# Performance work log

Hardware: AMD Instinct MI355X
Metric: run time of the kernel (lower is better)

## Reference

```python
import jax, jax.numpy as jnp
import numpy as np

H, DN, DR, DV = 16, 128, 64, 128   # heads, nope dim, rope dim, v dim
QR, KR = 1536, 512                 # q / kv lora ranks
HI, DI, TOPK = 32, 128, 512        # indexer heads, indexer head dim, index_topk

def rmsnorm(x, w, eps=1e-6):
    return x * jax.lax.rsqrt(jnp.mean(x * x, -1, keepdims=True) + eps) * w

def layernorm(x, w, b, eps=1e-5):
    m = jnp.mean(x, -1, keepdims=True)
    v = jnp.mean((x - m) ** 2, -1, keepdims=True)
    return (x - m) * jax.lax.rsqrt(v + eps) * w + b

def rope_interleaved(x, cos, sin):
    # x: [b,s,h,d]; cos,sin: [s,d//2]; pairs are (x[2j], x[2j+1])
    x0, x1 = x[..., 0::2], x[..., 1::2]
    c, s = cos[None, :, None, :], sin[None, :, None, :]
    return jnp.stack([x0 * c - x1 * s, x0 * s + x1 * c], -1).reshape(x.shape)

def rope_half(x, cos, sin):
    # non-interleaved variant: pairs are (x[j], x[j+d/2]); output = [real_half, imag_half]
    d = x.shape[-1] // 2
    x0, x1 = x[..., :d], x[..., d:]
    c, s = cos[None, :, None, :], sin[None, :, None, :]
    return jnp.concatenate([x0 * c - x1 * s, x0 * s + x1 * c], -1)

def setup_inputs():
    key = jax.random.key(0)
    B, S, DM = 1, 2048, 2048
    ks = jax.random.split(key, 10)
    w = lambda k, shape: jax.random.normal(k, shape, jnp.float32) * 0.02
    inp = {
        'hidden_states': jax.random.normal(ks[0], (B, S, DM), jnp.float32),
        'wq_a': w(ks[1], (QR, DM)),
        'q_norm_w': jnp.ones((QR,), jnp.float32),
        'wq_b': w(ks[2], (H * (DN + DR), QR)),
        'wkv_a': w(ks[3], (KR + DR, DM)),
        'kv_norm_w': jnp.ones((KR,), jnp.float32),
        'wkv_b': w(ks[4], (H * (DN + DV), KR)),
        'wo': w(ks[5], (DM, H * DV)),
        'idx_wq_b': w(ks[6], (HI * DI, QR)),
        'idx_wk': w(ks[7], (DI, DM)),
        'idx_kn_w': jnp.ones((DI,), jnp.float32),
        'idx_kn_b': jnp.zeros((DI,), jnp.float32),
        'idx_wproj': w(ks[8], (HI, DM)),
    }
    ang = jnp.arange(S, dtype=jnp.float32)[:, None] / (10000.0 ** (jnp.arange(0, DR, 2, dtype=jnp.float32) / DR))[None, :]
    inp['freqs_cos'], inp['freqs_sin'] = jnp.cos(ang), jnp.sin(ang)
    inp['mask'] = jnp.broadcast_to(
        jnp.where(jnp.tril(jnp.ones((S, S), bool)), 0.0, -jnp.inf).astype(jnp.float32), (B, S, S))
    return inp

def reference(hidden_states, freqs_cos, freqs_sin, mask, wq_a, q_norm_w, wq_b, wkv_a,
              kv_norm_w, wkv_b, wo, idx_wq_b, idx_wk, idx_kn_w, idx_kn_b, idx_wproj):
    B, S, DM = hidden_states.shape
    # --- MLA low-rank Q/KV projections ---
    qr = rmsnorm(hidden_states @ wq_a.T, q_norm_w)                       # [B,S,QR]
    q = (qr @ wq_b.T).reshape(B, S, H, DN + DR)
    q_pe = rope_interleaved(q[..., DN:], freqs_cos, freqs_sin)
    q = jnp.concatenate([q[..., :DN], q_pe], -1)                         # [B,S,H,192]
    kv_all = hidden_states @ wkv_a.T                                     # [B,S,KR+DR]
    kv = rmsnorm(kv_all[..., :KR], kv_norm_w)
    k_pe = rope_interleaved(kv_all[..., KR:][:, :, None, :], freqs_cos, freqs_sin)  # [B,S,1,DR]
    kvp = (kv @ wkv_b.T).reshape(B, S, H, DN + DV)
    k = jnp.concatenate([kvp[..., :DN], jnp.broadcast_to(k_pe, (B, S, H, DR))], -1)
    v = kvp[..., DN:]                                                    # [B,S,H,DV]
    scores = jnp.einsum('bshd,bthd->bsht', q, k) * (DN + DR) ** -0.5
    # --- indexer: relu-weighted scores -> top-k token set ---
    qi = (qr @ idx_wq_b.T).reshape(B, S, HI, DI)
    qi = jnp.concatenate([rope_half(qi[..., :DR], freqs_cos, freqs_sin), qi[..., DR:]], -1)
    ki = layernorm(hidden_states @ idx_wk.T, idx_kn_w, idx_kn_b)         # [B,S,DI]
    ki_pe = rope_half(ki[..., :DR][:, :, None, :], freqs_cos, freqs_sin)[:, :, 0, :]
    ki = jnp.concatenate([ki_pe, ki[..., DR:]], -1)
    wts = (hidden_states @ idx_wproj.T) * HI ** -0.5                     # [B,S,HI]
    iscores = jax.nn.relu(jnp.einsum('bshd,btd->bsht', qi, ki) * DI ** -0.5) * wts[..., None]
    index_scores = iscores.sum(2) + mask                                 # [B,S,S]
    topk_idx = jax.lax.top_k(index_scores, TOPK)[1]                      # [B,S,TOPK]
    index_mask = jnp.full((B, S, S), -jnp.inf, jnp.float32)
    index_mask = index_mask.at[jnp.arange(B)[:, None, None],
                               jnp.arange(S)[None, :, None], topk_idx].set(0.0)
    # --- sparse-masked attention ---
    scores = scores + (index_mask + mask)[:, :, None, :]
    probs = jax.nn.softmax(scores, axis=-1)
    out = jnp.einsum('bsht,bthd->bshd', probs, v).reshape(B, S, H * DV)
    return out @ wo.T
```

## Files before the change

kernel.cpp:

```cpp
#include <hip/hip_runtime.h>
#include <stdint.h>

typedef unsigned int uint;
typedef unsigned short u16;
typedef unsigned long long u64;

typedef float  f32x4 __attribute__((ext_vector_type(4)));
typedef uint   u32x4 __attribute__((ext_vector_type(4)));
typedef u16    u16x4 __attribute__((ext_vector_type(4)));
typedef u16    u16x8 __attribute__((ext_vector_type(8)));
typedef __bf16 bf16x8 __attribute__((ext_vector_type(8)));

#define DEV static __device__ __forceinline__
#define MFMA(a,b,c) __builtin_amdgcn_mfma_f32_16x16x32_bf16((a),(b),(c),0,0,0)
#define GLDS(src,dst) __builtin_amdgcn_global_load_lds((const __attribute__((address_space(1))) void*)(src),(__attribute__((address_space(3))) void*)(dst),16,0,0)

DEV u16 f2bf(float x){ union{float f;uint u;} v; v.f=x; return (u16)((v.u + 0x7fffu + ((v.u>>16)&1u))>>16); }
DEV float bf2f(u16 b){ union{uint u;float f;} v; v.u=((uint)b)<<16; return v.f; }
DEV int imin(int a,int b){ return a<b?a:b; }

__global__ void cvt_all(
    const float* __restrict__ hs, const float* __restrict__ wqa, const float* __restrict__ iwqb,
    const float* __restrict__ iwk, const float* __restrict__ iwp,
    const float* __restrict__ wqbw, const float* __restrict__ wkva, const float* __restrict__ wkvb,
    const float* __restrict__ wow,
    u16* __restrict__ hid_hi, u16* __restrict__ hid_lo, u16* __restrict__ wqa_hi, u16* __restrict__ wqa_lo,
    u16* __restrict__ iwqb_hi, u16* __restrict__ iwqb_lo, u16* __restrict__ kiwp_hi, u16* __restrict__ kiwp_lo,
    u16* __restrict__ wqb_b, u16* __restrict__ wkva_b, u16* __restrict__ wkvb_b, u16* __restrict__ wo_b)
{
  int i = blockIdx.x*blockDim.x + threadIdx.x;
  int st = gridDim.x*blockDim.x;
  for(; i < 6537216; i += st){
    const float* src; u16 *dh, *dl=nullptr; int j; bool split;
    if(i < 1048576){ src=hs;   dh=hid_hi;  dl=hid_lo;  j=i;         split=true; }
    else if(i < 1835008){ src=wqa;  dh=wqa_hi;  dl=wqa_lo;  j=i-1048576; split=true; }
    else if(i < 3407872){ src=iwqb; dh=iwqb_hi; dl=iwqb_lo; j=i-1835008; split=true; }
    else if(i < 3473408){ src=iwk;  dh=kiwp_hi; dl=kiwp_lo; j=i-3407872; split=true; }
    else if(i < 3489792){ src=iwp;  dh=kiwp_hi+128*2048; dl=kiwp_lo+128*2048; j=i-3473408; split=true; }
    else if(i < 4669440){ src=wqbw; dh=wqb_b;  j=i-3489792; split=false; }
    else if(i < 4964352){ src=wkva; dh=wkva_b; j=i-4669440; split=false; }
    else if(i < 5488640){ src=wkvb; dh=wkvb_b; j=i-4964352; split=false; }
    else               { src=wow;  dh=wo_b;   j=i-5488640; split=false; }
    f32x4 x = reinterpret_cast<const f32x4*>(src)[j];
    u16x4 h;
    #pragma unroll
    for(int k=0;k<4;k++) h[k]=f2bf(x[k]);
    reinterpret_cast<u16x4*>(dh)[j]=h;
    if(split){
      u16x4 l;
      #pragma unroll
      for(int k=0;k<4;k++) l[k]=f2bf(x[k]-bf2f(h[k]));
      reinterpret_cast<u16x4*>(dl)[j]=l;
    }
  }
}

template<int BK>
DEV void stageT(const u16* __restrict__ gbase, int ld, int row0, int maxrow, int k0, u16* lds){
  int tid = threadIdx.x, w = tid>>6, l = tid&63;
  if(BK==32){
    #pragma unroll
    for(int j=0;j<2;j++){
      int seg = w + j*4;
      int row = seg*16 + (l>>2);
      int gr = row0 + row; if(gr > maxrow) gr = maxrow;
      GLDS(gbase + (size_t)gr*ld + k0 + (l&3)*8, lds + seg*512);
    }
  } else {
    #pragma unroll
    for(int j=0;j<4;j++){
      int c = w + j*4;
      int row = c*8 + (l>>3);
      int gr = row0 + row; if(gr > maxrow) gr = maxrow;
      GLDS(gbase + (size_t)gr*ld + k0 + (l&7)*8, lds + c*512);
    }
  }
}

template<int SPLIT, int BK>
__global__ __launch_bounds__(256,2) void gemm_glds(
    const u16* __restrict__ Ah, const u16* __restrict__ Al, int lda,
    const u16* __restrict__ Bh, const u16* __restrict__ Bl, int ldb,
    float* __restrict__ C, int ldc, int M, int N, int K)
{
  __shared__ u16 sAh[128*BK];
  __shared__ u16 sBh[128*BK];
  __shared__ u16 sAl[SPLIT?128*BK:8];
  __shared__ u16 sBl[SPLIT?128*BK:8];
  const int tid = threadIdx.x;
  const int w = tid>>6, l = tid&63;
  const int wr = w>>1, wc = w&1;
  const int l15 = l&15, l16 = l>>4;

  int gx = gridDim.x;
  int nwg = gx*gridDim.y;
  int orig = blockIdx.x + gx*blockIdx.y;
  int qq = nwg>>3, rr = nwg&7, xc = orig&7, oo = orig>>3;
  int wg = (xc<rr ? xc*(qq+1) : rr*(qq+1)+(xc-rr)*qq) + oo;
  int m0 = (wg/gx)*128, n0 = (wg%gx)*128;

  int kz = K/(int)gridDim.z;
  int kbeg = blockIdx.z*kz;

  f32x4 acc[4][4];
  #pragma unroll
  for(int m=0;m<4;m++)
    #pragma unroll
    for(int n=0;n<4;n++) acc[m][n] = f32x4{0.f,0.f,0.f,0.f};

  for(int k0=kbeg; k0<kbeg+kz; k0+=BK){
    __syncthreads();
    stageT<BK>(Ah, lda, m0, M-1, k0, sAh);
    stageT<BK>(Bh, ldb, n0, N-1, k0, sBh);
    if(SPLIT){
      stageT<BK>(Al, lda, m0, M-1, k0, sAl);
      stageT<BK>(Bl, ldb, n0, N-1, k0, sBl);
    }
    asm volatile("s_waitcnt vmcnt(0)" ::: "memory");
    __syncthreads();
    #pragma unroll
    for(int kk=0;kk<BK/32;kk++){
      bf16x8 ah[4], bh[4];
      #pragma unroll
      for(int m=0;m<4;m++) ah[m] = *reinterpret_cast<const bf16x8*>(&sAh[(wr*64+m*16+l15)*BK + kk*32 + l16*8]);
      #pragma unroll
      for(int n=0;n<4;n++) bh[n] = *reinterpret_cast<const bf16x8*>(&sBh[(wc*64+n*16+l15)*BK + kk*32 + l16*8]);
      #pragma unroll
      for(int m=0;m<4;m++)
        #pragma unroll
        for(int n=0;n<4;n++) acc[m][n] = MFMA(ah[m], bh[n], acc[m][n]);
      if(SPLIT){
        bf16x8 t[4];
        #pragma unroll
        for(int n=0;n<4;n++) t[n] = *reinterpret_cast<const bf16x8*>(&sBl[(wc*64+n*16+l15)*BK + kk*32 + l16*8]);
        #pragma unroll
        for(int m=0;m<4;m++)
          #pragma unroll
          for(int n=0;n<4;n++) acc[m][n] = MFMA(ah[m], t[n], acc[m][n]);
        #pragma unroll
        for(int m=0;m<4;m++) t[m] = *reinterpret_cast<const bf16x8*>(&sAl[(wr*64+m*16+l15)*BK + kk*32 + l16*8]);
        #pragma unroll
        for(int m=0;m<4;m++)
          #pragma unroll
          for(int n=0;n<4;n++) acc[m][n] = MFMA(t[m], bh[n], acc[m][n]);
      }
    }
  }
  float* Cp = C + (size_t)blockIdx.z*M*ldc;
  #pragma unroll
  for(int m=0;m<4;m++){
    int row = m0 + wr*64 + m*16 + l16*4;
    #pragma unroll
    for(int n=0;n<4;n++){
      int col = n0 + wc*64 + n*16 + l15;
      if(col < N){
        #pragma unroll
        for(int r=0;r<4;r++){
          int rrow = row + r;
          if(rrow < M) Cp[(size_t)rrow*ldc + col] = acc[m][n][r];
        }
      }
    }
  }
}

__global__ __launch_bounds__(256) void rmsnorm_qr_split(
    const float* __restrict__ in, const float* __restrict__ w,
    u16* __restrict__ hi, u16* __restrict__ lo)
{
  int s = blockIdx.x, tid = threadIdx.x;
  __shared__ float red[4];
  const float* x = in + (size_t)s*1536;
  const size_t plane = 2048ull*1536;
  float xv[6]; float ss=0.f;
  #pragma unroll
  for(int i=0;i<6;i++){ int c = tid+i*256; xv[i] = x[c] + x[plane+c]; ss += xv[i]*xv[i]; }
  #pragma unroll
  for(int o=32;o>0;o>>=1) ss += __shfl_down(ss,o,64);
  if((tid&63)==0) red[tid>>6]=ss;
  __syncthreads();
  float total = red[0]+red[1]+red[2]+red[3];
  float scale = rsqrtf(total*(1.0f/1536.0f) + 1e-6f);
  #pragma unroll
  for(int i=0;i<6;i++){
    int c = tid + i*256;
    float vv = xv[i]*scale*w[c];
    u16 hv = f2bf(vv);
    hi[(size_t)s*1536+c]=hv;
    lo[(size_t)s*1536+c]=f2bf(vv - bf2f(hv));
  }
}

__global__ __launch_bounds__(256) void kv_norm_rope(
    const float* __restrict__ kva, const float* __restrict__ w,
    const float* __restrict__ fcos, const float* __restrict__ fsin,
    u16* __restrict__ kvb, float* __restrict__ kpe)
{
  int s = blockIdx.x, tid = threadIdx.x;
  __shared__ float red[4];
  const size_t plane = 2048ull*576;
  float xv[2]={0.f,0.f};
  #pragma unroll
  for(int c=0;c<4;c++){
    const float* xp = kva + (size_t)c*plane + (size_t)s*576;
    xv[0]+=xp[tid]; xv[1]+=xp[tid+256];
  }
  float ss = xv[0]*xv[0]+xv[1]*xv[1];
  #pragma unroll
  for(int o=32;o>0;o>>=1) ss += __shfl_down(ss,o,64);
  if((tid&63)==0) red[tid>>6]=ss;
  __syncthreads();
  float total = red[0]+red[1]+red[2]+red[3];
  float scale = rsqrtf(total*(1.0f/512.0f)+1e-6f);
  #pragma unroll
  for(int i=0;i<2;i++){ int c=tid+i*256; kvb[(size_t)s*512+c]=f2bf(xv[i]*scale*w[c]); }
  if(tid<32){
    float x0=0.f, x1=0.f;
    #pragma unroll
    for(int c=0;c<4;c++){
      const float* xp = kva + (size_t)c*plane + (size_t)s*576;
      x0 += xp[512+2*tid]; x1 += xp[513+2*tid];
    }
    float c0=fcos[(size_t)s*32+tid], s_=fsin[(size_t)s*32+tid];
    kpe[(size_t)s*64+2*tid]   = x0*c0 - x1*s_;
    kpe[(size_t)s*64+2*tid+1] = x0*s_ + x1*c0;
  }
}

__global__ __launch_bounds__(256) void rope_q_cvt(const float* __restrict__ qpre,
    const float* __restrict__ fcos, const float* __restrict__ fsin, u16* __restrict__ qb)
{
  int s = blockIdx.x;
  const float* rowp = qpre + (size_t)s*3072;
  u16* op = qb + (size_t)s*3072;
  for(int idx=threadIdx.x; idx<3072; idx+=256){
    int hh = idx/192, d = idx - hh*192;
    float vv;
    if(d < 128) vv = rowp[hh*192 + d];
    else{
      int i2 = (d-128)>>1;
      float c0 = fcos[(size_t)s*32+i2], s_ = fsin[(size_t)s*32+i2];
      float x0 = rowp[hh*192 + 128 + 2*i2], x1 = rowp[hh*192 + 129 + 2*i2];
      vv = ((d&1)==0) ? (x0*c0 - x1*s_) : (x0*s_ + x1*c0);
    }
    op[idx] = f2bf(vv);
  }
}

__global__ __launch_bounds__(256) void qi_rope_split(const float* __restrict__ qpre,
    const float* __restrict__ fcos, const float* __restrict__ fsin,
    u16* __restrict__ hi, u16* __restrict__ lo)
{
  int s = blockIdx.x;
  const float* rowp = qpre + (size_t)s*4096;
  for(int idx=threadIdx.x; idx<4096; idx+=256){
    int hh = idx>>7, d = idx&127;
    const float* hb = rowp + (hh<<7);
    float vv;
    if(d<32){ float c0=fcos[(size_t)s*32+d], s_=fsin[(size_t)s*32+d]; vv = hb[d]*c0 - hb[d+32]*s_; }
    else if(d<64){ int i2=d-32; float c0=fcos[(size_t)s*32+i2], s_=fsin[(size_t)s*32+i2]; vv = hb[i2]*s_ + hb[d]*c0; }
    else vv = hb[d];
    u16 hv = f2bf(vv);
    hi[(size_t)s*4096+idx]=hv;
    lo[(size_t)s*4096+idx]=f2bf(vv - bf2f(hv));
  }
}

__global__ __launch_bounds__(128) void ki_ln_rope_split(
    const float* __restrict__ kpre, const float* __restrict__ w, const float* __restrict__ bb,
    const float* __restrict__ fcos, const float* __restrict__ fsin,
    u16* __restrict__ hi, u16* __restrict__ lo, float* __restrict__ wts_out)
{
  int s = blockIdx.x, tid = threadIdx.x;
  __shared__ float red[2];
  __shared__ float ybuf[128];
  const size_t plane = 2048ull*160;
  float x = 0.f;
  #pragma unroll
  for(int c=0;c<8;c++) x += kpre[(size_t)c*plane + (size_t)s*160 + tid];
  if(tid<32){
    float ws = 0.f;
    #pragma unroll
    for(int c=0;c<8;c++) ws += kpre[(size_t)c*plane + (size_t)s*160 + 128 + tid];
    wts_out[(size_t)s*160 + 128 + tid] = ws;
  }
  float v = x;
  #pragma unroll
  for(int o=32;o>0;o>>=1) v += __shfl_down(v,o,64);
  if((tid&63)==0) red[tid>>6]=v;
  __syncthreads();
  float mean = (red[0]+red[1])*(1.f/128.f);
  __syncthreads();
  float dx = x - mean;
  v = dx*dx;
  #pragma unroll
  for(int o=32;o>0;o>>=1) v += __shfl_down(v,o,64);
  if((tid&63)==0) red[tid>>6]=v;
  __syncthreads();
  float var = (red[0]+red[1])*(1.f/128.f);
  float y = dx*rsqrtf(var+1e-5f)*w[tid] + bb[tid];
  ybuf[tid]=y;
  __syncthreads();
  float r;
  if(tid<32){ float c0=fcos[(size_t)s*32+tid], s_=fsin[(size_t)s*32+tid]; r = ybuf[tid]*c0 - ybuf[tid+32]*s_; }
  else if(tid<64){ int i2=tid-32; float c0=fcos[(size_t)s*32+i2], s_=fsin[(size_t)s*32+i2]; r = ybuf[i2]*s_ + ybuf[tid]*c0; }
  else r = y;
  u16 hv=f2bf(r);
  hi[(size_t)s*128+tid]=hv;
  lo[(size_t)s*128+tid]=f2bf(r-bf2f(hv));
}

__global__ __launch_bounds__(256) void transpose_assemble(const float* __restrict__ kvp,
    const float* __restrict__ kpe, u16* __restrict__ vt, u16* __restrict__ kb){
  __shared__ u16 T[64*136];
  int s0 = blockIdx.x*64, h = blockIdx.y;
  int tid = threadIdx.x;
  for(int idx=tid; idx<64*192; idx+=256){
    int r = idx/192, d = idx - r*192;
    float val = (d<128) ? kvp[(size_t)(s0+r)*4096 + h*256 + d] : kpe[(size_t)(s0+r)*64 + (d-128)];
    kb[((size_t)(s0+r)*16 + h)*192 + d] = f2bf(val);
  }
  #pragma unroll
  for(int i=0;i<8;i++){
    int ch = i*256 + tid;
    int r = ch>>5, cc = ch&31;
    f32x4 x = *reinterpret_cast<const f32x4*>(&kvp[(size_t)(s0+r)*4096 + h*256 + 128 + cc*4]);
    u16x4 y;
    #pragma unroll
    for(int j=0;j<4;j++) y[j] = f2bf(x[j]);
    *reinterpret_cast<u16x4*>(&T[r*136 + cc*4]) = y;
  }
  __syncthreads();
  #pragma unroll
  for(int i=0;i<4;i++){
    int ch = i*256 + tid;
    int d = ch>>3, sc = ch&7;
    u16x8 y;
    #pragma unroll
    for(int j=0;j<8;j++) y[j] = T[(sc*8+j)*136 + d];
    *reinterpret_cast<u16x8*>(&vt[((size_t)h*128 + d)*2048 + s0 + sc*8]) = y;
  }
}

DEV void isc_pass128(const u16* __restrict__ Q, const u16* __restrict__ Kb,
                     f32x4 (&sc)[4][2], int wm, int wn, int l15, int l16){
  #pragma unroll
  for(int ks=0;ks<4;ks++){
    bf16x8 a[4], b[2];
    #pragma unroll
    for(int m=0;m<4;m++){
      int row = wm*64 + m*16 + l15;
      a[m] = *reinterpret_cast<const bf16x8*>(&Q[row*128 + ((((ks<<2)+l16) ^ (row&7))<<3)]);
    }
    #pragma unroll
    for(int n=0;n<2;n++){
      int row = wn*32 + n*16 + l15;
      b[n] = *reinterpret_cast<const bf16x8*>(&Kb[row*128 + ((((ks<<2)+l16) ^ (row&7))<<3)]);
    }
    #pragma unroll
    for(int m=0;m<4;m++)
      #pragma unroll
      for(int n=0;n<2;n++) sc[m][n] = MFMA(a[m], b[n], sc[m][n]);
  }
}

__global__ __launch_bounds__(512,2) void idx_scores6(
    const u16* __restrict__ qih, const u16* __restrict__ qil,
    const u16* __restrict__ kih, const u16* __restrict__ kil,
    const float* __restrict__ wts,
    float* __restrict__ p0, float* __restrict__ p1, float* __restrict__ p2, float* __restrict__ p3)
{
  __shared__ u16 Kh[128*128];
  __shared__ u16 Kl[128*128];
  __shared__ u16 Qb[2][128*128];
  __shared__ float Wl[128*9];
  int orig = blockIdx.x;
  int bid = (orig&7)*68 + (orig>>3);
  int tileIdx = bid>>2, hg = bid&3;
  int si=0, t=tileIdx;
  while(t >= si+1){ t -= si+1; si++; }
  int s0 = si*128, t0 = t*128;
  float* plane = (hg==0)?p0:(hg==1)?p1:(hg==2)?p2:p3;
  float* outp = plane + (size_t)tileIdx*16384;
  int h0 = hg*8;
  int tid=threadIdx.x, w=tid>>6, l=tid&63;
  int wm=w>>2, wn=w&3, l15=l&15, l16=l>>4;
  const float cscale = 0.015625f;
  #pragma unroll
  for(int rnd=0;rnd<4;rnd++){
    int cid = rnd*512 + w*64 + l;
    int row = cid>>4, cc = cid&15;
    int scc = cc ^ (row&7);
    GLDS(kih + (size_t)(t0+row)*128 + scc*8, Kh + rnd*4096 + w*512);
    GLDS(kil + (size_t)(t0+row)*128 + scc*8, Kl + rnd*4096 + w*512);
  }
  #pragma unroll
  for(int rnd=0;rnd<4;rnd++){
    int cid = rnd*512 + w*64 + l;
    int row = cid>>4, cc = cid&15;
    int scc = cc ^ (row&7);
    GLDS(qih + (size_t)(s0+row)*4096 + h0*128 + scc*8, Qb[0] + rnd*4096 + w*512);
  }
  #pragma unroll
  for(int it=0;it<2;it++){
    int idx = it*512 + tid;
    int row = idx>>3, hh = idx&7;
    Wl[row*9+hh] = wts[(size_t)(s0+row)*160 + 128 + h0 + hh]*cscale;
  }
  asm volatile("s_waitcnt vmcnt(0)" ::: "memory");
  __syncthreads();
  f32x4 accI[4][2], sc[4][2];
  #pragma unroll
  for(int m=0;m<4;m++) for(int n=0;n<2;n++) accI[m][n] = f32x4{0.f,0.f,0.f,0.f};
  for(int s=0;s<16;s++){
    int nxt = s+1;
    if(nxt < 16){
      const u16* src = (nxt&1) ? qil : qih;
      int hh = h0 + (nxt>>1);
      u16* dst = Qb[nxt&1];
      #pragma unroll
      for(int rnd=0;rnd<4;rnd++){
        int cid = rnd*512 + w*64 + l;
        int row = cid>>4, cc = cid&15;
        int scc = cc ^ (row&7);
        GLDS(src + (size_t)(s0+row)*4096 + hh*128 + scc*8, dst + rnd*4096 + w*512);
      }
    }
    const u16* Q = Qb[s&1];
    if((s&1)==0){
      #pragma unroll
      for(int m=0;m<4;m++) for(int n=0;n<2;n++) sc[m][n] = f32x4{0.f,0.f,0.f,0.f};
      isc_pass128(Q, Kh, sc, wm, wn, l15, l16);
      isc_pass128(Q, Kl, sc, wm, wn, l15, l16);
    } else {
      isc_pass128(Q, Kh, sc, wm, wn, l15, l16);
      int hh = s>>1;
      #pragma unroll
      for(int m=0;m<4;m++)
        #pragma unroll
        for(int r=0;r<4;r++){
          float wv = Wl[(wm*64+m*16+l16*4+r)*9 + hh];
          #pragma unroll
          for(int n=0;n<2;n++) accI[m][n][r] += fmaxf(sc[m][n][r],0.f)*wv;
        }
    }
    asm volatile("s_waitcnt vmcnt(0)" ::: "memory");
    __syncthreads();
  }
  #pragma unroll
  for(int m=0;m<4;m++)
    #pragma unroll
    for(int n=0;n<2;n++)
      #pragma unroll
      for(int r=0;r<4;r++)
        outp[(wm*64+m*16+l16*4+r)*128 + wn*32 + n*16 + l15] = accI[m][n][r];
}

DEV uint fkey(float f){ union{float f;uint u;} v; v.f=f; return (v.u & 0x80000000u) ? ~v.u : (v.u | 0x80000000u); }

__global__ __launch_bounds__(256) void topk_mask(
    const float* __restrict__ p0, const float* __restrict__ p1,
    const float* __restrict__ p2, const float* __restrict__ p3, u64* __restrict__ bits)
{
  int s = blockIdx.x;
  int n = s+1;
  int tid = threadIdx.x;
  if(n <= 512){
    for(int wI=tid; wI<32; wI+=256){
      u64 m=0; int base=wI*64;
      if(base < n){ int cnt=n-base; m = (cnt>=64)? ~0ull : ((1ull<<cnt)-1ull); }
      bits[(size_t)s*32+wI]=m;
    }
    return;
  }
  __shared__ float row[2048];
  __shared__ uint hist[256];
  __shared__ uint sh_B, sh_k;
  __shared__ uint wcnt[32];
  int si = s>>7, sr = s&127;
  size_t triBase = (size_t)(si*(si+1)/2);
  for(int c=tid; c<n; c+=256){
    size_t off = (triBase + (size_t)(c>>7))*16384 + (size_t)sr*128 + (c&127);
    row[c] = p0[off]+p1[off]+p2[off]+p3[off];
  }
  __syncthreads();
  uint prefix=0, k=512;
  for(int shift=24; shift>=0; shift-=8){
    hist[tid]=0;
    __syncthreads();
    for(int t2=tid;t2<n;t2+=256){
      uint u = fkey(row[t2]);
      bool ok = (shift==24) || ((u>>(shift+8)) == (prefix>>(shift+8)));
      if(ok) atomicAdd(&hist[(u>>shift)&255u],1u);
    }
    __syncthreads();
    for(int offd=1; offd<256; offd<<=1){
      uint add = (tid+offd<256)? hist[tid+offd] : 0u;
      __syncthreads();
      hist[tid] += add;
      __syncthreads();
    }
    uint nxtv = (tid<255)? hist[tid+1] : 0u;
    if(hist[tid]>=k && nxtv<k){ sh_B=(uint)tid; sh_k = k - nxtv; }
    __syncthreads();
    prefix |= sh_B<<shift;
    k = sh_k;
    __syncthreads();
  }
  uint thr = prefix;
  if(tid<32) wcnt[tid]=0;
  __syncthreads();
  int nw = (n+63)>>6;
  if(tid < nw){
    int base=tid*64, end = base+64; if(end>n) end=n;
    uint c=0;
    for(int t2=base;t2<end;t2++) if(fkey(row[t2])==thr) c++;
    wcnt[tid]=c;
  }
  __syncthreads();
  if(tid==0){
    uint runv=0;
    for(int i=0;i<32;i++){ uint c=wcnt[i]; wcnt[i]=runv; runv+=c; }
  }
  __syncthreads();
  if(tid<32){
    u64 m=0; int base=tid*64;
    if(base<n){
      uint rank = wcnt[tid];
      int end = base+64; if(end>n) end=n;
      for(int t2=base;t2<end;t2++){
        uint u = fkey(row[t2]);
        if(u>thr) m |= (1ull<<(t2-base));
        else if(u==thr){ if(rank<k) m |= (1ull<<(t2-base)); rank++; }
      }
    }
    bits[(size_t)s*32+tid]=m;
  }
}

__global__ __launch_bounds__(256,3) void flash_attn(
    const u16* __restrict__ q, const u16* __restrict__ k, const u16* __restrict__ vt,
    const u64* __restrict__ bits, u16* __restrict__ o,
    u16* __restrict__ Opart, float* __restrict__ ml)
{
  __shared__ u16 Ks[64*192];
  __shared__ u16 Vt[128*64];
  __shared__ u16 Pl[64*72];
  int h = blockIdx.y;
  int pp = blockIdx.x;
  int sblk=0, chunk=0;
  for(int i=0;i<32;i++){
    int sb = 31-i; int ncc = (sb>>3)+1;
    if(pp < ncc){ sblk=sb; chunk=pp; break; }
    pp -= ncc;
  }
  int nc = (sblk>>3)+1, ntiles = sblk+1, s0 = sblk*64;
  int tid=threadIdx.x, w=tid>>6, l=tid&63;
  int l15=l&15, l16=l>>4;
  const float sscale = 0.07216878364870323f;
  bf16x8 qf[6];
  #pragma unroll
  for(int ks=0;ks<6;ks++)
    qf[ks] = *reinterpret_cast<const bf16x8*>(&q[((size_t)(s0+w*16+l15)*16 + h)*192 + ks*32 + l16*8]);
  f32x4 Oa[8];
  #pragma unroll
  for(int n=0;n<8;n++) Oa[n] = f32x4{0.f,0.f,0.f,0.f};
  float mrun[4], lrun[4];
  #pragma unroll
  for(int r=0;r<4;r++){ mrun[r]=-__builtin_inff(); lrun[r]=0.f; }
  int tt0 = chunk*8, tt1 = imin(tt0+8, ntiles);
  for(int tt=tt0; tt<tt1; tt++){
    int t0 = tt*64;
    __syncthreads();
    #pragma unroll
    for(int rnd=0;rnd<6;rnd++){
      int cid = rnd*256 + w*64 + l;
      int row = cid/24, cc = cid - row*24;
      int scc = cc ^ (row&7);
      GLDS(k + ((size_t)(t0+row)*16 + h)*192 + scc*8, Ks + rnd*2048 + w*512);
    }
    #pragma unroll
    for(int rnd=0;rnd<4;rnd++){
      int cid = rnd*256 + w*64 + l;
      int row = cid>>3, cc = cid&7;
      int scc = cc ^ (row&7);
      GLDS(vt + ((size_t)h*128 + row)*2048 + t0 + scc*8, Vt + rnd*2048 + w*512);
    }
    asm volatile("s_waitcnt vmcnt(0)" ::: "memory");
    __syncthreads();
    f32x4 S[4];
    #pragma unroll
    for(int n=0;n<4;n++) S[n] = f32x4{0.f,0.f,0.f,0.f};
    #pragma unroll
    for(int ks=0;ks<6;ks++){
      bf16x8 b[4];
      #pragma unroll
      for(int n=0;n<4;n++){
        int row = n*16+l15;
        b[n] = *reinterpret_cast<const bf16x8*>(&Ks[row*192 + ((((ks<<2)+l16) ^ (row&7))<<3)]);
      }
      #pragma unroll
      for(int n=0;n<4;n++) S[n] = MFMA(qf[ks], b[n], S[n]);
    }
    #pragma unroll
    for(int r=0;r<4;r++){
      int srow = s0 + w*16 + l16*4 + r;
      u64 wrd = bits[(size_t)srow*32 + (t0>>6)];
      float mx = -__builtin_inff();
      #pragma unroll
      for(int n=0;n<4;n++){
        int bitp = n*16 + l15;
        int tcol = t0 + bitp;
        bool ok = (tcol <= srow) && ((wrd>>bitp)&1ull);
        float val = ok ? S[n][r]*sscale : -__builtin_inff();
        S[n][r] = val;
        mx = fmaxf(mx, val);
      }
      #pragma unroll
      for(int off=1;off<16;off<<=1) mx = fmaxf(mx, __shfl_xor(mx, off, 64));
      float mold = mrun[r];
      float mnew = fmaxf(mold, mx);
      bool inf0 = (mnew == -__builtin_inff());
      float alpha = inf0 ? 1.f : __expf(mold - mnew);
      float rs = 0.f;
      #pragma unroll
      for(int n=0;n<4;n++){
        float p = inf0 ? 0.f : __expf(S[n][r] - mnew);
        S[n][r] = p;
        rs += p;
      }
      #pragma unroll
      for(int off=1;off<16;off<<=1) rs += __shfl_xor(rs, off, 64);
      mrun[r]=mnew;
      lrun[r] = lrun[r]*alpha + rs;
      #pragma unroll
      for(int n=0;n<8;n++) Oa[n][r] *= alpha;
    }
    #pragma unroll
    for(int n=0;n<4;n++)
      #pragma unroll
      for(int r=0;r<4;r++)
        Pl[(w*16+l16*4+r)*72 + n*16+l15] = f2bf(S[n][r]);
    #pragma unroll
    for(int ks=0;ks<2;ks++){
      bf16x8 a = *reinterpret_cast<const bf16x8*>(&Pl[(w*16+l15)*72 + ks*32 + l16*8]);
      bf16x8 bb[8];
      #pragma unroll
      for(int n=0;n<8;n++){
        int d = n*16+l15;
        bb[n] = *reinterpret_cast<const bf16x8*>(&Vt[d*64 + ((((ks<<2)+l16) ^ (d&7))<<3)]);
      }
      #pragma unroll
      for(int n=0;n<8;n++) Oa[n] = MFMA(a, bb[n], Oa[n]);
    }
  }
  if(nc == 1){
    #pragma unroll
    for(int r=0;r<4;r++){
      int srow = s0 + w*16 + l16*4 + r;
      float inv = 1.f/lrun[r];
      #pragma unroll
      for(int n=0;n<8;n++)
        o[(size_t)srow*2048 + h*128 + n*16 + l15] = f2bf(Oa[n][r]*inv);
    }
  } else {
    int part = ((h*32 + sblk)<<2) + chunk;
    u16* Op = Opart + (size_t)part*8192;
    #pragma unroll
    for(int r=0;r<4;r++){
      int rit = w*16 + l16*4 + r;
      #pragma unroll
      for(int n=0;n<8;n++)
        Op[rit*128 + n*16 + l15] = f2bf(Oa[n][r]);
      if(l15==0){
        ml[(size_t)part*128 + rit*2]   = mrun[r];
        ml[(size_t)part*128 + rit*2+1] = lrun[r];
      }
    }
  }
}

__global__ __launch_bounds__(256) void flash_combine(
    const u16* __restrict__ Opart, const float* __restrict__ ml, u16* __restrict__ o)
{
  int b = blockIdx.x;
  int h = b/24, sblk = 8 + (b%24);
  int nc = (sblk>>3)+1;
  int tid = threadIdx.x;
  int r = tid>>2, dq = (tid&3)*32;
  int s0 = sblk*64;
  int pbase = (h*32+sblk)<<2;
  float m[4], lv[4], wgt[4];
  float M = -__builtin_inff();
  for(int c=0;c<nc;c++){
    m[c]  = ml[(size_t)(pbase+c)*128 + r*2];
    lv[c] = ml[(size_t)(pbase+c)*128 + r*2 + 1];
    if(lv[c] > 0.f) M = fmaxf(M, m[c]);
  }
  float L = 0.f;
  for(int c=0;c<nc;c++){
    wgt[c] = (lv[c] > 0.f) ? __expf(m[c]-M) : 0.f;
    L += lv[c]*wgt[c];
  }
  float inv = 1.f/L;
  for(int dd=0; dd<32; dd+=8){
    float accv[8];
    #pragma unroll
    for(int j=0;j<8;j++) accv[j]=0.f;
    for(int c=0;c<nc;c++){
      u16x8 pv = *reinterpret_cast<const u16x8*>(&Opart[(size_t)(pbase+c)*8192 + r*128 + dq + dd]);
      #pragma unroll
      for(int j=0;j<8;j++) accv[j] += wgt[c]*bf2f(pv[j]);
    }
    u16x8 ov;
    #pragma unroll
    for(int j=0;j<8;j++) ov[j] = f2bf(accv[j]*inv);
    *reinterpret_cast<u16x8*>(&o[(size_t)(s0+r)*2048 + h*128 + dq + dd]) = ov;
  }
}

extern "C" void kernel_launch(void* const* d_in, const int* in_sizes, int n_in,
                              void* d_out, int out_size, void* d_ws, size_t ws_size,
                              hipStream_t stream)
{
  (void)in_sizes; (void)n_in; (void)out_size;
  const float* hs   = (const float*)d_in[0];
  const float* wqa  = (const float*)d_in[1];
  const float* qnw  = (const float*)d_in[2];
  const float* wqbw = (const float*)d_in[3];
  const float* wkva = (const float*)d_in[4];
  const float* kvnw = (const float*)d_in[5];
  const float* wkvb = (const float*)d_in[6];
  const float* wow  = (const float*)d_in[7];
  const float* iwqb = (const float*)d_in[8];
  const float* iwk  = (const float*)d_in[9];
  const float* iknw = (const float*)d_in[10];
  const float* iknb = (const float*)d_in[11];
  const float* iwp  = (const float*)d_in[12];
  const float* fcos = (const float*)d_in[13];
  const float* fsin = (const float*)d_in[14];
  float* outp = (float*)d_out;

  char* base = (char*)d_ws;
  size_t off = 0;
  auto alloc = [&](size_t bytes)->char*{ char* p = base+off; off += (bytes+255)&~(size_t)255; return p; };
  u16* hid_hi = (u16*)alloc(2048ull*2048*2);
  u16* hid_lo = (u16*)alloc(2048ull*2048*2);
  u16* wqa_hi = (u16*)alloc(1536ull*2048*2);
  u16* wqa_lo = (u16*)alloc(1536ull*2048*2);
  u16* wqb_b  = (u16*)alloc(3072ull*1536*2);
  u16* wkva_b = (u16*)alloc(576ull*2048*2);
  u16* wkvb_b = (u16*)alloc(4096ull*512*2);
  u16* wo_b   = (u16*)alloc(2048ull*2048*2);
  u16* iwqb_hi= (u16*)alloc(4096ull*1536*2);
  u16* iwqb_lo= (u16*)alloc(4096ull*1536*2);
  u16* kiwp_hi= (u16*)alloc(160ull*2048*2);
  u16* kiwp_lo= (u16*)alloc(160ull*2048*2);
  float* kiwp_C=(float*)alloc(2048ull*160*4);
  u16* qr_hi  = (u16*)alloc(2048ull*1536*2);
  u16* qr_lo  = (u16*)alloc(2048ull*1536*2);
  u16* kv_b   = (u16*)alloc(2048ull*512*2);
  float* kpe  = (float*)alloc(2048ull*64*4);
  u16* k_b    = (u16*)alloc(2048ull*16*192*2);
  u16* v_t    = (u16*)alloc(16ull*128*2048*2);
  u16* ki_hi  = (u16*)alloc(2048ull*128*2);
  u16* ki_lo  = (u16*)alloc(2048ull*128*2);
  u64* bits   = (u64*)alloc(2048ull*32*8);
  u16* attn_b = (u16*)alloc(2048ull*2048*2);
  float* reg1 = (float*)alloc(2048ull*4096*4);
  if(ws_size < off) return;

  u16* q_b      = wqa_hi;
  u16* qi_hi    = hid_hi;
  u16* qi_lo    = iwqb_hi;
  float* ml     = (float*)qr_lo;
  float* qr_pre = reg1;
  float* q_pre  = reg1;
  float* kva_part = reg1;
  float* kvp    = reg1;
  float* kiwp_part = reg1;
  float* qi_pre = reg1;
  const size_t PLANE = 136ull*16384;
  float* ip0 = reg1;
  float* ip1 = reg1 + PLANE;
  float* ip2 = reg1 + 2*PLANE;
  float* ip3 = (float*)wqb_b;
  u16* Opart = (u16*)reg1;

  auto G1 = [&](const u16* A,int lda,const u16* B,int ldb,float* C,int ldc,int M,int N,int K,int z){
    dim3 g((unsigned)((N+127)/128), (unsigned)((M+127)/128), (unsigned)z);
    gemm_glds<0,64><<<g,256,0,stream>>>(A,nullptr,lda,B,nullptr,ldb,C,ldc,M,N,K);
  };
  auto G3 = [&](const u16* Ah,const u16* Al,int lda,const u16* Bh,const u16* Bl,int ldb,float* C,int ldc,int M,int N,int K,int z){
    dim3 g((unsigned)((N+127)/128), (unsigned)((M+127)/128), (unsigned)z);
    gemm_glds<1,32><<<g,256,0,stream>>>(Ah,Al,lda,Bh,Bl,ldb,C,ldc,M,N,K);
  };

  cvt_all<<<2048,256,0,stream>>>(hs,wqa,iwqb,iwk,iwp,wqbw,wkva,wkvb,wow,
      hid_hi,hid_lo,wqa_hi,wqa_lo,iwqb_hi,iwqb_lo,kiwp_hi,kiwp_lo,
      wqb_b,wkva_b,wkvb_b,wo_b);

  G3(hid_hi,hid_lo,2048, wqa_hi,wqa_lo,2048, qr_pre,1536, 2048,1536,2048, 2);
  rmsnorm_qr_split<<<2048,256,0,stream>>>(qr_pre, qnw, qr_hi, qr_lo);

  G1(qr_hi,1536, wqb_b,1536, q_pre,3072, 2048,3072,1536, 1);
  rope_q_cvt<<<2048,256,0,stream>>>(q_pre, fcos, fsin, q_b);

  G1(hid_hi,2048, wkva_b,2048, kva_part,576, 2048,576,2048, 4);
  kv_norm_rope<<<2048,256,0,stream>>>(kva_part, kvnw, fcos, fsin, kv_b, kpe);
  G1(kv_b,512, wkvb_b,512, kvp,4096, 2048,4096,512, 1);
  transpose_assemble<<<dim3(32,16),256,0,stream>>>(kvp, kpe, v_t, k_b);

  G3(hid_hi,hid_lo,2048, kiwp_hi,kiwp_lo,2048, kiwp_part,160, 2048,160,2048, 8);
  ki_ln_rope_split<<<2048,128,0,stream>>>(kiwp_part, iknw, iknb, fcos, fsin, ki_hi, ki_lo, kiwp_C);

  G3(qr_hi,qr_lo,1536, iwqb_hi,iwqb_lo,1536, qi_pre,4096, 2048,4096,1536, 1);
  qi_rope_split<<<2048,256,0,stream>>>(qi_pre, fcos, fsin, qi_hi, qi_lo);

  idx_scores6<<<544,512,0,stream>>>(qi_hi, qi_lo, ki_hi, ki_lo, kiwp_C, ip0, ip1, ip2, ip3);
  topk_mask<<<2048,256,0,stream>>>(ip0, ip1, ip2, ip3, bits);

  flash_attn<<<dim3(80,16),256,0,stream>>>(q_b, k_b, v_t, bits, attn_b, Opart, ml);
  flash_combine<<<384,256,0,stream>>>(Opart, ml, attn_b);
  G1(attn_b,2048, wo_b,2048, outp,2048, 2048,2048,2048, 1);
}
```

Before: 554.6 us.

## Halve indexer score tile rows and drop Q double buffering to raise occupancy

The indexer score kernel now uses 64-row query tiles instead of 128, doubling the grid and halving per-wave accumulators. It uses a single Q shared buffer instead of two and reads head weights straight from global memory instead of staging them in shared memory. Together these cut LDS and register use so four blocks can fit per CU instead of two. The cost is lost overlap of Q loads with compute, an extra barrier per step, and reloading each K tile twice as often. The causal tile enumeration and the topk reader's partial-plane indexing are updated to match the new tiling.

```diff
diff --git a/kernel.cpp b/kernel.cpp
--- a/kernel.cpp
+++ b/kernel.cpp
@@ -342,14 +342,14 @@
   }
 }
 
-DEV void isc_pass128(const u16* __restrict__ Q, const u16* __restrict__ Kb,
-                     f32x4 (&sc)[4][2], int wm, int wn, int l15, int l16){
+DEV void isc_pass64(const u16* __restrict__ Q, const u16* __restrict__ Kb,
+                    f32x4 (&sc)[2][2], int wm, int wn, int l15, int l16){
   #pragma unroll
   for(int ks=0;ks<4;ks++){
-    bf16x8 a[4], b[2];
-    #pragma unroll
-    for(int m=0;m<4;m++){
-      int row = wm*64 + m*16 + l15;
+    bf16x8 a[2], b[2];
+    #pragma unroll
+    for(int m=0;m<2;m++){
+      int row = wm*32 + m*16 + l15;
       a[m] = *reinterpret_cast<const bf16x8*>(&Q[row*128 + ((((ks<<2)+l16) ^ (row&7))<<3)]);
     }
     #pragma unroll
@@ -358,13 +358,13 @@
       b[n] = *reinterpret_cast<const bf16x8*>(&Kb[row*128 + ((((ks<<2)+l16) ^ (row&7))<<3)]);
     }
     #pragma unroll
-    for(int m=0;m<4;m++)
+    for(int m=0;m<2;m++)
       #pragma unroll
       for(int n=0;n<2;n++) sc[m][n] = MFMA(a[m], b[n], sc[m][n]);
   }
 }
 
-__global__ __launch_bounds__(512,2) void idx_scores6(
+__global__ __launch_bounds__(512,4) void idx_scores7(
     const u16* __restrict__ qih, const u16* __restrict__ qil,
     const u16* __restrict__ kih, const u16* __restrict__ kil,
     const float* __restrict__ wts,
@@ -372,16 +372,16 @@
 {
   __shared__ u16 Kh[128*128];
   __shared__ u16 Kl[128*128];
-  __shared__ u16 Qb[2][128*128];
-  __shared__ float Wl[128*9];
+  __shared__ u16 Qb[64*128];
   int orig = blockIdx.x;
-  int bid = (orig&7)*68 + (orig>>3);
+  int bid = (orig&7)*136 + (orig>>3);
   int tileIdx = bid>>2, hg = bid&3;
   int si=0, t=tileIdx;
-  while(t >= si+1){ t -= si+1; si++; }
-  int s0 = si*128, t0 = t*128;
+  #pragma unroll 1
+  for(; si<32; si++){ int cnt=(si+2)>>1; if(t<cnt) break; t-=cnt; }
+  int s0 = si*64, t0 = t*128;
   float* plane = (hg==0)?p0:(hg==1)?p1:(hg==2)?p2:p3;
-  float* outp = plane + (size_t)tileIdx*16384;
+  float* outp = plane + (size_t)tileIdx*8192;
   int h0 = hg*8;
   int tid=threadIdx.x, w=tid>>6, l=tid&63;
   int wm=w>>2, wn=w&3, l15=l&15, l16=l>>4;
@@ -395,65 +395,59 @@
     GLDS(kil + (size_t)(t0+row)*128 + scc*8, Kl + rnd*4096 + w*512);
   }
   #pragma unroll
-  for(int rnd=0;rnd<4;rnd++){
+  for(int rnd=0;rnd<2;rnd++){
     int cid = rnd*512 + w*64 + l;
     int row = cid>>4, cc = cid&15;
     int scc = cc ^ (row&7);
-    GLDS(qih + (size_t)(s0+row)*4096 + h0*128 + scc*8, Qb[0] + rnd*4096 + w*512);
-  }
-  #pragma unroll
-  for(int it=0;it<2;it++){
-    int idx = it*512 + tid;
-    int row = idx>>3, hh = idx&7;
-    Wl[row*9+hh] = wts[(size_t)(s0+row)*160 + 128 + h0 + hh]*cscale;
+    GLDS(qih + (size_t)(s0+row)*4096 + h0*128 + scc*8, Qb + rnd*4096 + w*512);
   }
   asm volatile("s_waitcnt vmcnt(0)" ::: "memory");
   __syncthreads();
-  f32x4 accI[4][2], sc[4][2];
-  #pragma unroll
-  for(int m=0;m<4;m++) for(int n=0;n<2;n++) accI[m][n] = f32x4{0.f,0.f,0.f,0.f};
+  f32x4 accI[2][2], sc[2][2];
+  #pragma unroll
+  for(int m=0;m<2;m++) for(int n=0;n<2;n++) accI[m][n] = f32x4{0.f,0.f,0.f,0.f};
   for(int s=0;s<16;s++){
+    const u16* Q = Qb;
+    if((s&1)==0){
+      #pragma unroll
+      for(int m=0;m<2;m++) for(int n=0;n<2;n++) sc[m][n] = f32x4{0.f,0.f,0.f,0.f};
+      isc_pass64(Q, Kh, sc, wm, wn, l15, l16);
+      isc_pass64(Q, Kl, sc, wm, wn, l15, l16);
+    } else {
+      isc_pass64(Q, Kh, sc, wm, wn, l15, l16);
+      int hh = h0 + (s>>1);
+      #pragma unroll
+      for(int m=0;m<2;m++)
+        #pragma unroll
+        for(int r=0;r<4;r++){
+          float wv = wts[(size_t)(s0+wm*32+m*16+l16*4+r)*160 + 128 + hh]*cscale;
+          #pragma unroll
+          for(int n=0;n<2;n++) accI[m][n][r] += fmaxf(sc[m][n][r],0.f)*wv;
+        }
+    }
+    __syncthreads();
     int nxt = s+1;
     if(nxt < 16){
       const u16* src = (nxt&1) ? qil : qih;
       int hh = h0 + (nxt>>1);
-      u16* dst = Qb[nxt&1];
-      #pragma unroll
-      for(int rnd=0;rnd<4;rnd++){
+      #pragma unroll
+      for(int rnd=0;rnd<2;rnd++){
         int cid = rnd*512 + w*64 + l;
         int row = cid>>4, cc = cid&15;
         int scc = cc ^ (row&7);
-        GLDS(src + (size_t)(s0+row)*4096 + hh*128 + scc*8, dst + rnd*4096 + w*512);
+        GLDS(src + (size_t)(s0+row)*4096 + hh*128 + scc*8, Qb + rnd*4096 + w*512);
       }
-    }
-    const u16* Q = Qb[s&1];
-    if((s&1)==0){
-      #pragma unroll
-      for(int m=0;m<4;m++) for(int n=0;n<2;n++) sc[m][n] = f32x4{0.f,0.f,0.f,0.f};
-      isc_pass128(Q, Kh, sc, wm, wn, l15, l16);
-      isc_pass128(Q, Kl, sc, wm, wn, l15, l16);
-    } else {
-      isc_pass128(Q, Kh, sc, wm, wn, l15, l16);
-      int hh = s>>1;
-      #pragma unroll
-      for(int m=0;m<4;m++)
-        #pragma unroll
-        for(int r=0;r<4;r++){
-          float wv = Wl[(wm*64+m*16+l16*4+r)*9 + hh];
-          #pragma unroll
-          for(int n=0;n<2;n++) accI[m][n][r] += fmaxf(sc[m][n][r],0.f)*wv;
-        }
-    }
-    asm volatile("s_waitcnt vmcnt(0)" ::: "memory");
-    __syncthreads();
-  }
-  #pragma unroll
-  for(int m=0;m<4;m++)
+      asm volatile("s_waitcnt vmcnt(0)" ::: "memory");
+      __syncthreads();
+    }
+  }
+  #pragma unroll
+  for(int m=0;m<2;m++)
     #pragma unroll
     for(int n=0;n<2;n++)
       #pragma unroll
       for(int r=0;r<4;r++)
-        outp[(wm*64+m*16+l16*4+r)*128 + wn*32 + n*16 + l15] = accI[m][n][r];
+        outp[(wm*32+m*16+l16*4+r)*128 + wn*32 + n*16 + l15] = accI[m][n][r];
 }
 
 DEV uint fkey(float f){ union{float f;uint u;} v; v.f=f; return (v.u & 0x80000000u) ? ~v.u : (v.u | 0x80000000u); }
@@ -477,10 +471,10 @@
   __shared__ uint hist[256];
   __shared__ uint sh_B, sh_k;
   __shared__ uint wcnt[32];
-  int si = s>>7, sr = s&127;
-  size_t triBase = (size_t)(si*(si+1)/2);
+  int si = s>>6, sr = s&63;
+  size_t triBase = (size_t)(((si+1)*(si+1))>>2);
   for(int c=tid; c<n; c+=256){
-    size_t off = (triBase + (size_t)(c>>7))*16384 + (size_t)sr*128 + (c&127);
+    size_t off = (triBase + (size_t)(c>>7))*8192 + (size_t)sr*128 + (c&127);
     row[c] = p0[off]+p1[off]+p2[off]+p3[off];
   }
   __syncthreads();
@@ -780,7 +774,7 @@
   float* kvp    = reg1;
   float* kiwp_part = reg1;
   float* qi_pre = reg1;
-  const size_t PLANE = 136ull*16384;
+  const size_t PLANE = 272ull*8192;
   float* ip0 = reg1;
   float* ip1 = reg1 + PLANE;
   float* ip2 = reg1 + 2*PLANE;
@@ -817,7 +811,7 @@
   G3(qr_hi,qr_lo,1536, iwqb_hi,iwqb_lo,1536, qi_pre,4096, 2048,4096,1536, 1);
   qi_rope_split<<<2048,256,0,stream>>>(qi_pre, fcos, fsin, qi_hi, qi_lo);
 
-  idx_scores6<<<544,512,0,stream>>>(qi_hi, qi_lo, ki_hi, ki_lo, kiwp_C, ip0, ip1, ip2, ip3);
+  idx_scores7<<<1088,512,0,stream>>>(qi_hi, qi_lo, ki_hi, ki_lo, kiwp_C, ip0, ip1, ip2, ip3);
   topk_mask<<<2048,256,0,stream>>>(ip0, ip1, ip2, ip3, bits);
 
   flash_attn<<<dim3(80,16),256,0,stream>>>(q_b, k_b, v_t, bits, attn_b, Opart, ml);
```

Measured after the change: 532.7 us. 1.04x faster.
